# Kernel tuning notes

Hardware: AMD Instinct MI355X
Metric: run time of the kernel (lower is better)

The kernel has to match this reference:

```python
import jax, jax.numpy as jnp
import numpy as np

N, E, IN, HID, CLS = 40000, 640000, 128, 256, 40
K = 2  # SGConv k hops

def setup_inputs() -> dict:
    key = jax.random.key(0)
    ks = jax.random.split(key, 5)
    features = jax.random.normal(ks[0], (N, IN), dtype=jnp.float32)
    src = jax.random.randint(ks[1], (E,), 0, N)
    dst = jax.random.randint(ks[2], (E,), 0, N)
    # SGConv fc: in_feats -> n_hidden
    W1 = jax.random.normal(ks[3], (IN, HID), dtype=jnp.float32) / np.float32(np.sqrt(IN))
    b1 = jnp.zeros((HID,), dtype=jnp.float32)
    # model-level linear: n_hidden -> n_classes
    W2 = jax.random.normal(ks[4], (HID, CLS), dtype=jnp.float32) / np.float32(np.sqrt(HID))
    b2 = jnp.zeros((CLS,), dtype=jnp.float32)
    return {"features": features, "src": src, "dst": dst,
            "W1": W1, "b1": b1, "W2": W2, "b2": b2}

def reference(features, src, dst, W1, b1, W2, b2):
    # symmetric degree norm (DGL SGConv: in-degree, clamp min=1)
    deg = jax.ops.segment_sum(jnp.ones((E,), jnp.float32), dst, num_segments=N)
    norm = jax.lax.rsqrt(jnp.maximum(deg, 1.0))[:, None]  # [N,1]
    h = features
    for _ in range(K):
        h = h * norm
        h = jax.ops.segment_sum(h[src], dst, num_segments=N)  # A @ h via edge scatter
        h = h * norm
    h = h @ W1 + b1            # SGConv fc
    return jax.nn.relu(h) @ W2 + b2  # model relu + linear
```

## Files before the change

### kernel.cpp

```cpp
#include <hip/hip_runtime.h>

#define N_NODES 40000
#define N_EDGES 640000
#define IN_F 128
#define HID_F 256
#define CLS_F 40
#define CLS_P 48
#define MB 32
#define TS_LD 264

typedef __attribute__((ext_vector_type(8))) short bf16x8;
typedef __attribute__((ext_vector_type(4))) float f32x4;
typedef __attribute__((ext_vector_type(4))) _Float16 half4;
typedef __attribute__((ext_vector_type(8))) _Float16 half8;

#define MFMA(a, b, c) __builtin_amdgcn_mfma_f32_16x16x32_bf16(a, b, c, 0, 0, 0)

__device__ __forceinline__ unsigned short f32_to_bf16_rne(float f) {
    unsigned int u = __float_as_uint(f);
    unsigned int r = u + 0x7fffu + ((u >> 16) & 1u);
    return (unsigned short)(r >> 16);
}


__global__ void k_count(const int* __restrict__ dst, int* __restrict__ counts) {
    int e = blockIdx.x * blockDim.x + threadIdx.x;
    if (e < N_EDGES) atomicAdd(&counts[dst[e]], 1);
}

__global__ void k_scan1(const int* __restrict__ counts, int* __restrict__ bsum) {
    __shared__ int s[256];
    int i = blockIdx.x * 256 + threadIdx.x;
    s[threadIdx.x] = (i < N_NODES) ? counts[i] : 0;
    __syncthreads();
    for (int off = 128; off > 0; off >>= 1) {
        if (threadIdx.x < off) s[threadIdx.x] += s[threadIdx.x + off];
        __syncthreads();
    }
    if (threadIdx.x == 0) bsum[blockIdx.x] = s[0];
}

__global__ void k_scan2(int* __restrict__ bsum, int nb) {
    __shared__ int s[256];
    int t = threadIdx.x;
    int v = (t < nb) ? bsum[t] : 0;
    s[t] = v;
    __syncthreads();
    for (int off = 1; off < 256; off <<= 1) {
        int x = (t >= off) ? s[t - off] : 0;
        __syncthreads();
        s[t] += x;
        __syncthreads();
    }
    if (t < nb) bsum[t] = s[t] - v;
}

__global__ void k_scan3(const int* __restrict__ counts, const int* __restrict__ bsum,
                        int* __restrict__ rowptr, int* __restrict__ cursor) {
    __shared__ int s[256];
    int t = threadIdx.x;
    int i = blockIdx.x * 256 + t;
    int v = (i < N_NODES) ? counts[i] : 0;
    s[t] = v;
    __syncthreads();
    for (int off = 1; off < 256; off <<= 1) {
        int x = (t >= off) ? s[t - off] : 0;
        __syncthreads();
        s[t] += x;
        __syncthreads();
    }
    if (i < N_NODES) {
        int excl = s[t] - v + bsum[blockIdx.x];
        rowptr[i] = excl;
        cursor[i] = excl;
    }
}

__global__ void k_norm(const int* __restrict__ counts,
                       float* __restrict__ norm, float* __restrict__ norm2) {
    int i = blockIdx.x * blockDim.x + threadIdx.x;
    if (i < N_NODES) {
        float d = (float)counts[i];
        float r = rsqrtf(fmaxf(d, 1.0f));
        norm[i] = r;
        norm2[i] = r * r;
    }
}

__global__ void k_fill(const int* __restrict__ src, const int* __restrict__ dst,
                       int* __restrict__ cursor, unsigned short* __restrict__ csr_src) {
    int e = blockIdx.x * blockDim.x + threadIdx.x;
    if (e < N_EDGES) {
        int d = dst[e];
        int p = atomicAdd(&cursor[d], 1);
        csr_src[p] = (unsigned short)src[e];
    }
}


__global__ __launch_bounds__(256) void k_scale(
        const float* __restrict__ f, const float* __restrict__ norm,
        _Float16* __restrict__ xs) {
    int i = blockIdx.x * 256 + threadIdx.x;
    float s = norm[i >> 4];
    float4 a = ((const float4*)f)[i * 2];
    float4 b = ((const float4*)f)[i * 2 + 1];
    half8 h;
    h[0] = (_Float16)(a.x * s); h[1] = (_Float16)(a.y * s);
    h[2] = (_Float16)(a.z * s); h[3] = (_Float16)(a.w * s);
    h[4] = (_Float16)(b.x * s); h[5] = (_Float16)(b.y * s);
    h[6] = (_Float16)(b.z * s); h[7] = (_Float16)(b.w * s);
    ((half8*)xs)[i] = h;
}


#define HOP_GATHER16                                                          \
    int gid  = blockIdx.x * 8 + (threadIdx.x >> 5);                           \
    int lane = threadIdx.x & 31;                                              \
    if (gid >= N_NODES) return;                                               \
    int start = rowptr[gid];                                                  \
    int cnt   = counts[gid];                                                  \
    const _Float16* base = gin + lane * 4;                                    \
    float4 acc = make_float4(0.f, 0.f, 0.f, 0.f);                             \
    int i = 0;                                                                \
    for (; i + 3 < cnt; i += 4) {                                             \
        int s0 = csr_src[start + i];     int s1 = csr_src[start + i + 1];     \
        int s2 = csr_src[start + i + 2]; int s3 = csr_src[start + i + 3];     \
        half4 v0 = *(const half4*)(base + (size_t)s0 * IN_F);                 \
        half4 v1 = *(const half4*)(base + (size_t)s1 * IN_F);                 \
        half4 v2 = *(const half4*)(base + (size_t)s2 * IN_F);                 \
        half4 v3 = *(const half4*)(base + (size_t)s3 * IN_F);                 \
        acc.x += (float)v0[0] + (float)v1[0] + (float)v2[0] + (float)v3[0];   \
        acc.y += (float)v0[1] + (float)v1[1] + (float)v2[1] + (float)v3[1];   \
        acc.z += (float)v0[2] + (float)v1[2] + (float)v2[2] + (float)v3[2];   \
        acc.w += (float)v0[3] + (float)v1[3] + (float)v2[3] + (float)v3[3];   \
    }                                                                         \
    for (; i < cnt; i++) {                                                    \
        int s = csr_src[start + i];                                           \
        half4 v = *(const half4*)(base + (size_t)s * IN_F);                   \
        acc.x += (float)v[0]; acc.y += (float)v[1];                           \
        acc.z += (float)v[2]; acc.w += (float)v[3];                           \
    }

__global__ __launch_bounds__(256) void k_hop(
        const _Float16* __restrict__ gin, _Float16* __restrict__ gout,
        const unsigned short* __restrict__ csr_src, const int* __restrict__ rowptr,
        const int* __restrict__ counts, const float* __restrict__ oscale) {
    HOP_GATHER16
    float sc = oscale[gid];
    half4 o;
    o[0] = (_Float16)(acc.x * sc); o[1] = (_Float16)(acc.y * sc);
    o[2] = (_Float16)(acc.z * sc); o[3] = (_Float16)(acc.w * sc);
    *(half4*)(gout + (size_t)gid * IN_F + lane * 4) = o;
}

__global__ __launch_bounds__(256) void k_hop_split(
        const _Float16* __restrict__ gin,
        unsigned short* __restrict__ ghi, unsigned short* __restrict__ glo,
        const unsigned short* __restrict__ csr_src, const int* __restrict__ rowptr,
        const int* __restrict__ counts, const float* __restrict__ oscale) {
    HOP_GATHER16
    float sc = oscale[gid];
    float vv[4] = {acc.x * sc, acc.y * sc, acc.z * sc, acc.w * sc};
    ushort4 h, l;
    unsigned short* hp = (unsigned short*)&h;
    unsigned short* lp = (unsigned short*)&l;
    #pragma unroll
    for (int j = 0; j < 4; j++) {
        unsigned short hi = f32_to_bf16_rne(vv[j]);
        float fh = __uint_as_float((unsigned)hi << 16);
        hp[j] = hi;
        lp[j] = f32_to_bf16_rne(vv[j] - fh);
    }
    ((ushort4*)(ghi + (size_t)gid * IN_F))[lane] = h;
    ((ushort4*)(glo + (size_t)gid * IN_F))[lane] = l;
}


__global__ __launch_bounds__(256) void k_prep(
        const float* __restrict__ W1, const float* __restrict__ W2,
        unsigned short* __restrict__ w1hi, unsigned short* __restrict__ w1lo,
        unsigned short* __restrict__ w2hi, unsigned short* __restrict__ w2lo) {
    int idx = blockIdx.x * 256 + threadIdx.x;
    if (idx < IN_F * HID_F) {
        int k = idx >> 8;
        int c = idx & 255;
        float v = W1[idx];
        unsigned short hi = f32_to_bf16_rne(v);
        float fh = __uint_as_float((unsigned)hi << 16);
        unsigned short lo = f32_to_bf16_rne(v - fh);
        w1hi[c * IN_F + k] = hi;
        w1lo[c * IN_F + k] = lo;
    }
    int idx2 = idx - IN_F * HID_F;
    if (idx2 >= 0 && idx2 < CLS_P * HID_F) {
        int c = idx2 >> 8;
        int k = idx2 & 255;
        float v = (c < CLS_F) ? W2[k * CLS_F + c] : 0.f;
        unsigned short hi = f32_to_bf16_rne(v);
        float fh = __uint_as_float((unsigned)hi << 16);
        unsigned short lo = f32_to_bf16_rne(v - fh);
        w2hi[c * HID_F + k] = hi;
        w2lo[c * HID_F + k] = lo;
    }
}


#define LOAD_A(AH, AL, rt) do {                                              \
    const unsigned short* hp_ = h2hi + (size_t)(n0 + (rt) * 16 + lr) * IN_F + lg * 8; \
    const unsigned short* lp_ = h2lo + (size_t)(n0 + (rt) * 16 + lr) * IN_F + lg * 8; \
    _Pragma("unroll")                                                        \
    for (int kq = 0; kq < 4; kq++) {                                         \
        AH[kq] = *(const bf16x8*)(hp_ + kq * 32);                            \
        AL[kq] = *(const bf16x8*)(lp_ + kq * 32);                            \
    }                                                                        \
} while (0)

#define TILE(AH, AL, rt) do {                                                \
    _Pragma("unroll")                                                        \
    for (int ct = 0; ct < 4; ct++) {                                         \
        f32x4 acc = {0.f, 0.f, 0.f, 0.f};                                    \
        _Pragma("unroll")                                                    \
        for (int kq = 0; kq < 4; kq++) {                                     \
            acc = MFMA(AH[kq], b1h[ct][kq], acc);                            \
            acc = MFMA(AH[kq], b1l[ct][kq], acc);                            \
            acc = MFMA(AL[kq], b1h[ct][kq], acc);                            \
        }                                                                    \
        int col_ = w * 64 + ct * 16 + lr;                                    \
        _Pragma("unroll")                                                    \
        for (int r = 0; r < 4; r++) {                                        \
            int row_ = (rt) * 16 + lg * 4 + r;                               \
            float v_ = acc[r] + b1v[ct];                                     \
            v_ = v_ > 0.f ? v_ : 0.f;                                        \
            unsigned short hi_ = f32_to_bf16_rne(v_);                        \
            float fh_ = __uint_as_float((unsigned)hi_ << 16);                \
            tshi[row_ * TS_LD + col_] = hi_;                                 \
            tslo[row_ * TS_LD + col_] = f32_to_bf16_rne(v_ - fh_);           \
        }                                                                    \
    }                                                                        \
} while (0)

__global__ __launch_bounds__(256, 2) void k_mlp(
        const unsigned short* __restrict__ h2hi, const unsigned short* __restrict__ h2lo,
        const unsigned short* __restrict__ w1hi, const unsigned short* __restrict__ w1lo,
        const float* __restrict__ b1,
        const unsigned short* __restrict__ w2hi, const unsigned short* __restrict__ w2lo,
        const float* __restrict__ b2,
        float* __restrict__ out) {
    __shared__ __align__(16) unsigned short tshi[MB * TS_LD];
    __shared__ __align__(16) unsigned short tslo[MB * TS_LD];
    int n0 = blockIdx.x * MB;
    int t  = threadIdx.x;
    int w  = t >> 6;
    int l  = t & 63;
    int lr = l & 15;
    int lg = l >> 4;

    bf16x8 b1h[4][4], b1l[4][4];
    float  b1v[4];
    #pragma unroll
    for (int ct = 0; ct < 4; ct++) {
        int col = w * 64 + ct * 16 + lr;
        const unsigned short* bhp = w1hi + (size_t)col * IN_F + lg * 8;
        const unsigned short* blp = w1lo + (size_t)col * IN_F + lg * 8;
        #pragma unroll
        for (int kq = 0; kq < 4; kq++) {
            b1h[ct][kq] = *(const bf16x8*)(bhp + kq * 32);
            b1l[ct][kq] = *(const bf16x8*)(blp + kq * 32);
        }
        b1v[ct] = b1[col];
    }

    bf16x8 aAh[4], aAl[4], aBh[4], aBl[4];
    LOAD_A(aAh, aAl, 0);
    LOAD_A(aBh, aBl, 1);
    TILE(aAh, aAl, 0);
    TILE(aBh, aBl, 1);
    __syncthreads();

    if (w < 3) {
        int col = w * 16 + lr;
        bf16x8 b2h[8], b2l[8];
        const unsigned short* bhp = w2hi + (size_t)col * HID_F + lg * 8;
        const unsigned short* blp = w2lo + (size_t)col * HID_F + lg * 8;
        #pragma unroll
        for (int kk = 0; kk < 8; kk++) {
            b2h[kk] = *(const bf16x8*)(bhp + kk * 32);
            b2l[kk] = *(const bf16x8*)(blp + kk * 32);
        }
        float bias = (col < CLS_F) ? b2[col] : 0.f;
        #pragma unroll
        for (int rt2 = 0; rt2 < 2; rt2++) {
            const unsigned short* ahp = tshi + (rt2 * 16 + lr) * TS_LD + lg * 8;
            const unsigned short* alp = tslo + (rt2 * 16 + lr) * TS_LD + lg * 8;
            f32x4 acc0 = {0.f, 0.f, 0.f, 0.f};
            f32x4 acc1 = {0.f, 0.f, 0.f, 0.f};
            #pragma unroll
            for (int kk = 0; kk < 4; kk++) {
                bf16x8 a_h0 = *(const bf16x8*)(ahp + kk * 32);
                bf16x8 a_l0 = *(const bf16x8*)(alp + kk * 32);
                bf16x8 a_h1 = *(const bf16x8*)(ahp + (kk + 4) * 32);
                bf16x8 a_l1 = *(const bf16x8*)(alp + (kk + 4) * 32);
                acc0 = MFMA(a_h0, b2h[kk], acc0);
                acc1 = MFMA(a_h1, b2h[kk + 4], acc1);
                acc0 = MFMA(a_h0, b2l[kk], acc0);
                acc1 = MFMA(a_h1, b2l[kk + 4], acc1);
                acc0 = MFMA(a_l0, b2h[kk], acc0);
                acc1 = MFMA(a_l1, b2h[kk + 4], acc1);
            }
            if (col < CLS_F) {
                #pragma unroll
                for (int r = 0; r < 4; r++) {
                    int mrow = n0 + rt2 * 16 + lg * 4 + r;
                    out[(size_t)mrow * CLS_F + col] = acc0[r] + acc1[r] + bias;
                }
            }
        }
    }
}


extern "C" void kernel_launch(void* const* d_in, const int* in_sizes, int n_in,
                              void* d_out, int out_size, void* d_ws, size_t ws_size,
                              hipStream_t stream) {
    const float* features = (const float*)d_in[0];
    const int*   src      = (const int*)d_in[1];
    const int*   dst      = (const int*)d_in[2];
    const float* W1       = (const float*)d_in[3];
    const float* b1       = (const float*)d_in[4];
    const float* W2       = (const float*)d_in[5];
    const float* b2       = (const float*)d_in[6];
    float*       out      = (float*)d_out;

    char* ws = (char*)d_ws;
    size_t off = 0;
    auto alloc = [&](size_t bytes) -> void* {
        void* p = ws + off;
        off += (bytes + 255) & ~(size_t)255;
        return p;
    };
    int*   counts = (int*)alloc((size_t)N_NODES * 4);
    int*   rowptr = (int*)alloc((size_t)N_NODES * 4);
    int*   cursor = (int*)alloc((size_t)N_NODES * 4);
    int*   bsum   = (int*)alloc(256 * 4);
    float* norm   = (float*)alloc((size_t)N_NODES * 4);
    float* norm2  = (float*)alloc((size_t)N_NODES * 4);
    unsigned short* csr = (unsigned short*)alloc((size_t)N_EDGES * 2);
    _Float16* xs  = (_Float16*)alloc((size_t)N_NODES * IN_F * 2);
    _Float16* h1  = (_Float16*)alloc((size_t)N_NODES * IN_F * 2);
    unsigned short* h2hi = (unsigned short*)alloc((size_t)N_NODES * IN_F * 2);
    unsigned short* h2lo = (unsigned short*)alloc((size_t)N_NODES * IN_F * 2);
    unsigned short* w1hi = (unsigned short*)alloc((size_t)HID_F * IN_F * 2);
    unsigned short* w1lo = (unsigned short*)alloc((size_t)HID_F * IN_F * 2);
    unsigned short* w2hi = (unsigned short*)alloc((size_t)CLS_P * HID_F * 2);
    unsigned short* w2lo = (unsigned short*)alloc((size_t)CLS_P * HID_F * 2);

    hipMemsetAsync(counts, 0, (size_t)N_NODES * 4, stream);

    int nb = (N_NODES + 255) / 256;
    k_count<<<(N_EDGES + 255) / 256, 256, 0, stream>>>(dst, counts);
    k_prep<<<(IN_F * HID_F + CLS_P * HID_F + 255) / 256, 256, 0, stream>>>(
        W1, W2, w1hi, w1lo, w2hi, w2lo);
    k_scan1<<<nb, 256, 0, stream>>>(counts, bsum);
    k_scan2<<<1, 256, 0, stream>>>(bsum, nb);
    k_scan3<<<nb, 256, 0, stream>>>(counts, bsum, rowptr, cursor);
    k_norm<<<nb, 256, 0, stream>>>(counts, norm, norm2);
    k_fill<<<(N_EDGES + 255) / 256, 256, 0, stream>>>(src, dst, cursor, csr);

    k_scale<<<N_NODES * IN_F / 8 / 256, 256, 0, stream>>>(features, norm, xs);
    k_hop<<<(N_NODES + 7) / 8, 256, 0, stream>>>(xs, h1, csr, rowptr, counts, norm2);
    k_hop_split<<<(N_NODES + 7) / 8, 256, 0, stream>>>(h1, h2hi, h2lo, csr, rowptr,
                                                       counts, norm);

    k_mlp<<<N_NODES / MB, 256, 0, stream>>>(h2hi, h2lo, w1hi, w1lo, b1, w2hi, w2lo, b2, out);
}
```

Before: 237.6 us.

## Fuse second hop gather into MLP kernel and merge setup kernels

The second hop's gather and hi/lo bf16 split now run inside the MLP kernel. Results go to a swizzled LDS tile instead of round-tripping h2hi/h2lo through global memory. The norm computation is folded into the scan kernel, and edge fill, feature scaling and weight prep are merged into one multi-role launch. This removes several launches and about 20 MB of intermediate traffic. The risk is that the latency-bound gather now runs inside the MFMA kernel, which has higher register and LDS pressure and lower occupancy.

After: 262.5 us. 10.5% more time.

```diff
diff --git a/kernel.cpp b/kernel.cpp
--- a/kernel.cpp
+++ b/kernel.cpp
@@ -8,6 +8,7 @@
 #define CLS_P 48
 #define MB 32
 #define TS_LD 264
+#define A_LD 136
 
 typedef __attribute__((ext_vector_type(8))) short bf16x8;
 typedef __attribute__((ext_vector_type(4))) float f32x4;
@@ -20,6 +21,10 @@
     unsigned int u = __float_as_uint(f);
     unsigned int r = u + 0x7fffu + ((u >> 16) & 1u);
     return (unsigned short)(r >> 16);
+}
+
+__device__ __forceinline__ int aswz(int row, int col_us) {
+    return row * A_LD + (col_us ^ ((row & 7) << 3));
 }
 
 
@@ -55,8 +60,9 @@
     if (t < nb) bsum[t] = s[t] - v;
 }
 
-__global__ void k_scan3(const int* __restrict__ counts, const int* __restrict__ bsum,
-                        int* __restrict__ rowptr, int* __restrict__ cursor) {
+__global__ void k_scan3n(const int* __restrict__ counts, const int* __restrict__ bsum,
+                         int* __restrict__ rowptr, int* __restrict__ cursor,
+                         float* __restrict__ norm, float* __restrict__ norm2) {
     __shared__ int s[256];
     int t = threadIdx.x;
     int i = blockIdx.x * 256 + t;
@@ -73,80 +79,94 @@
         int excl = s[t] - v + bsum[blockIdx.x];
         rowptr[i] = excl;
         cursor[i] = excl;
-    }
-}
-
-__global__ void k_norm(const int* __restrict__ counts,
-                       float* __restrict__ norm, float* __restrict__ norm2) {
-    int i = blockIdx.x * blockDim.x + threadIdx.x;
-    if (i < N_NODES) {
-        float d = (float)counts[i];
+        float d = (float)v;
         float r = rsqrtf(fmaxf(d, 1.0f));
         norm[i] = r;
         norm2[i] = r * r;
     }
 }
 
-__global__ void k_fill(const int* __restrict__ src, const int* __restrict__ dst,
-                       int* __restrict__ cursor, unsigned short* __restrict__ csr_src) {
-    int e = blockIdx.x * blockDim.x + threadIdx.x;
-    if (e < N_EDGES) {
+
+__global__ __launch_bounds__(256) void k_fsp(
+        const int* __restrict__ src, const int* __restrict__ dst,
+        int* __restrict__ cursor, unsigned short* __restrict__ csr_src,
+        const float* __restrict__ features, const float* __restrict__ norm,
+        _Float16* __restrict__ xs,
+        const float* __restrict__ W1, const float* __restrict__ W2,
+        unsigned short* __restrict__ w1hi, unsigned short* __restrict__ w1lo,
+        unsigned short* __restrict__ w2hi, unsigned short* __restrict__ w2lo) {
+    int b = blockIdx.x;
+    if (b < 2500) {
+        int e = b * 256 + threadIdx.x;
         int d = dst[e];
         int p = atomicAdd(&cursor[d], 1);
         csr_src[p] = (unsigned short)src[e];
-    }
-}
-
-
-__global__ __launch_bounds__(256) void k_scale(
-        const float* __restrict__ f, const float* __restrict__ norm,
-        _Float16* __restrict__ xs) {
-    int i = blockIdx.x * 256 + threadIdx.x;
-    float s = norm[i >> 4];
-    float4 a = ((const float4*)f)[i * 2];
-    float4 b = ((const float4*)f)[i * 2 + 1];
-    half8 h;
-    h[0] = (_Float16)(a.x * s); h[1] = (_Float16)(a.y * s);
-    h[2] = (_Float16)(a.z * s); h[3] = (_Float16)(a.w * s);
-    h[4] = (_Float16)(b.x * s); h[5] = (_Float16)(b.y * s);
-    h[6] = (_Float16)(b.z * s); h[7] = (_Float16)(b.w * s);
-    ((half8*)xs)[i] = h;
-}
-
-
-#define HOP_GATHER16                                                          \
-    int gid  = blockIdx.x * 8 + (threadIdx.x >> 5);                           \
-    int lane = threadIdx.x & 31;                                              \
-    if (gid >= N_NODES) return;                                               \
-    int start = rowptr[gid];                                                  \
-    int cnt   = counts[gid];                                                  \
-    const _Float16* base = gin + lane * 4;                                    \
-    float4 acc = make_float4(0.f, 0.f, 0.f, 0.f);                             \
-    int i = 0;                                                                \
-    for (; i + 3 < cnt; i += 4) {                                             \
-        int s0 = csr_src[start + i];     int s1 = csr_src[start + i + 1];     \
-        int s2 = csr_src[start + i + 2]; int s3 = csr_src[start + i + 3];     \
-        half4 v0 = *(const half4*)(base + (size_t)s0 * IN_F);                 \
-        half4 v1 = *(const half4*)(base + (size_t)s1 * IN_F);                 \
-        half4 v2 = *(const half4*)(base + (size_t)s2 * IN_F);                 \
-        half4 v3 = *(const half4*)(base + (size_t)s3 * IN_F);                 \
-        acc.x += (float)v0[0] + (float)v1[0] + (float)v2[0] + (float)v3[0];   \
-        acc.y += (float)v0[1] + (float)v1[1] + (float)v2[1] + (float)v3[1];   \
-        acc.z += (float)v0[2] + (float)v1[2] + (float)v2[2] + (float)v3[2];   \
-        acc.w += (float)v0[3] + (float)v1[3] + (float)v2[3] + (float)v3[3];   \
-    }                                                                         \
-    for (; i < cnt; i++) {                                                    \
-        int s = csr_src[start + i];                                           \
-        half4 v = *(const half4*)(base + (size_t)s * IN_F);                   \
-        acc.x += (float)v[0]; acc.y += (float)v[1];                           \
-        acc.z += (float)v[2]; acc.w += (float)v[3];                           \
-    }
+    } else if (b < 5000) {
+        int i = (b - 2500) * 256 + threadIdx.x;
+        float s = norm[i >> 4];
+        float4 a = ((const float4*)features)[i * 2];
+        float4 c = ((const float4*)features)[i * 2 + 1];
+        half8 h;
+        h[0] = (_Float16)(a.x * s); h[1] = (_Float16)(a.y * s);
+        h[2] = (_Float16)(a.z * s); h[3] = (_Float16)(a.w * s);
+        h[4] = (_Float16)(c.x * s); h[5] = (_Float16)(c.y * s);
+        h[6] = (_Float16)(c.z * s); h[7] = (_Float16)(c.w * s);
+        ((half8*)xs)[i] = h;
+    } else {
+        int idx = (b - 5000) * 256 + threadIdx.x;
+        if (idx < IN_F * HID_F) {
+            int k = idx >> 8;
+            int c = idx & 255;
+            float v = W1[idx];
+            unsigned short hi = f32_to_bf16_rne(v);
+            float fh = __uint_as_float((unsigned)hi << 16);
+            w1hi[c * IN_F + k] = hi;
+            w1lo[c * IN_F + k] = f32_to_bf16_rne(v - fh);
+        }
+        int idx2 = idx - IN_F * HID_F;
+        if (idx2 >= 0 && idx2 < CLS_P * HID_F) {
+            int c = idx2 >> 8;
+            int k = idx2 & 255;
+            float v = (c < CLS_F) ? W2[k * CLS_F + c] : 0.f;
+            unsigned short hi = f32_to_bf16_rne(v);
+            float fh = __uint_as_float((unsigned)hi << 16);
+            w2hi[c * HID_F + k] = hi;
+            w2lo[c * HID_F + k] = f32_to_bf16_rne(v - fh);
+        }
+    }
+}
+
 
 __global__ __launch_bounds__(256) void k_hop(
         const _Float16* __restrict__ gin, _Float16* __restrict__ gout,
         const unsigned short* __restrict__ csr_src, const int* __restrict__ rowptr,
         const int* __restrict__ counts, const float* __restrict__ oscale) {
-    HOP_GATHER16
+    int gid  = blockIdx.x * 8 + (threadIdx.x >> 5);
+    int lane = threadIdx.x & 31;
+    if (gid >= N_NODES) return;
+    int start = rowptr[gid];
+    int cnt   = counts[gid];
+    const _Float16* base = gin + lane * 4;
+    float4 acc = make_float4(0.f, 0.f, 0.f, 0.f);
+    int i = 0;
+    for (; i + 3 < cnt; i += 4) {
+        int s0 = csr_src[start + i];     int s1 = csr_src[start + i + 1];
+        int s2 = csr_src[start + i + 2]; int s3 = csr_src[start + i + 3];
+        half4 v0 = *(const half4*)(base + (size_t)s0 * IN_F);
+        half4 v1 = *(const half4*)(base + (size_t)s1 * IN_F);
+        half4 v2 = *(const half4*)(base + (size_t)s2 * IN_F);
+        half4 v3 = *(const half4*)(base + (size_t)s3 * IN_F);
+        acc.x += (float)v0[0] + (float)v1[0] + (float)v2[0] + (float)v3[0];
+        acc.y += (float)v0[1] + (float)v1[1] + (float)v2[1] + (float)v3[1];
+        acc.z += (float)v0[2] + (float)v1[2] + (float)v2[2] + (float)v3[2];
+        acc.w += (float)v0[3] + (float)v1[3] + (float)v2[3] + (float)v3[3];
+    }
+    for (; i < cnt; i++) {
+        int s = csr_src[start + i];
+        half4 v = *(const half4*)(base + (size_t)s * IN_F);
+        acc.x += (float)v[0]; acc.y += (float)v[1];
+        acc.z += (float)v[2]; acc.w += (float)v[3];
+    }
     float sc = oscale[gid];
     half4 o;
     o[0] = (_Float16)(acc.x * sc); o[1] = (_Float16)(acc.y * sc);
@@ -154,99 +174,18 @@
     *(half4*)(gout + (size_t)gid * IN_F + lane * 4) = o;
 }
 
-__global__ __launch_bounds__(256) void k_hop_split(
-        const _Float16* __restrict__ gin,
-        unsigned short* __restrict__ ghi, unsigned short* __restrict__ glo,
+
+__global__ __launch_bounds__(256, 2) void k_mlp(
+        const _Float16* __restrict__ h1,
         const unsigned short* __restrict__ csr_src, const int* __restrict__ rowptr,
-        const int* __restrict__ counts, const float* __restrict__ oscale) {
-    HOP_GATHER16
-    float sc = oscale[gid];
-    float vv[4] = {acc.x * sc, acc.y * sc, acc.z * sc, acc.w * sc};
-    ushort4 h, l;
-    unsigned short* hp = (unsigned short*)&h;
-    unsigned short* lp = (unsigned short*)&l;
-    #pragma unroll
-    for (int j = 0; j < 4; j++) {
-        unsigned short hi = f32_to_bf16_rne(vv[j]);
-        float fh = __uint_as_float((unsigned)hi << 16);
-        hp[j] = hi;
-        lp[j] = f32_to_bf16_rne(vv[j] - fh);
-    }
-    ((ushort4*)(ghi + (size_t)gid * IN_F))[lane] = h;
-    ((ushort4*)(glo + (size_t)gid * IN_F))[lane] = l;
-}
-
-
-__global__ __launch_bounds__(256) void k_prep(
-        const float* __restrict__ W1, const float* __restrict__ W2,
-        unsigned short* __restrict__ w1hi, unsigned short* __restrict__ w1lo,
-        unsigned short* __restrict__ w2hi, unsigned short* __restrict__ w2lo) {
-    int idx = blockIdx.x * 256 + threadIdx.x;
-    if (idx < IN_F * HID_F) {
-        int k = idx >> 8;
-        int c = idx & 255;
-        float v = W1[idx];
-        unsigned short hi = f32_to_bf16_rne(v);
-        float fh = __uint_as_float((unsigned)hi << 16);
-        unsigned short lo = f32_to_bf16_rne(v - fh);
-        w1hi[c * IN_F + k] = hi;
-        w1lo[c * IN_F + k] = lo;
-    }
-    int idx2 = idx - IN_F * HID_F;
-    if (idx2 >= 0 && idx2 < CLS_P * HID_F) {
-        int c = idx2 >> 8;
-        int k = idx2 & 255;
-        float v = (c < CLS_F) ? W2[k * CLS_F + c] : 0.f;
-        unsigned short hi = f32_to_bf16_rne(v);
-        float fh = __uint_as_float((unsigned)hi << 16);
-        unsigned short lo = f32_to_bf16_rne(v - fh);
-        w2hi[c * HID_F + k] = hi;
-        w2lo[c * HID_F + k] = lo;
-    }
-}
-
-
-#define LOAD_A(AH, AL, rt) do {                                              \
-    const unsigned short* hp_ = h2hi + (size_t)(n0 + (rt) * 16 + lr) * IN_F + lg * 8; \
-    const unsigned short* lp_ = h2lo + (size_t)(n0 + (rt) * 16 + lr) * IN_F + lg * 8; \
-    _Pragma("unroll")                                                        \
-    for (int kq = 0; kq < 4; kq++) {                                         \
-        AH[kq] = *(const bf16x8*)(hp_ + kq * 32);                            \
-        AL[kq] = *(const bf16x8*)(lp_ + kq * 32);                            \
-    }                                                                        \
-} while (0)
-
-#define TILE(AH, AL, rt) do {                                                \
-    _Pragma("unroll")                                                        \
-    for (int ct = 0; ct < 4; ct++) {                                         \
-        f32x4 acc = {0.f, 0.f, 0.f, 0.f};                                    \
-        _Pragma("unroll")                                                    \
-        for (int kq = 0; kq < 4; kq++) {                                     \
-            acc = MFMA(AH[kq], b1h[ct][kq], acc);                            \
-            acc = MFMA(AH[kq], b1l[ct][kq], acc);                            \
-            acc = MFMA(AL[kq], b1h[ct][kq], acc);                            \
-        }                                                                    \
-        int col_ = w * 64 + ct * 16 + lr;                                    \
-        _Pragma("unroll")                                                    \
-        for (int r = 0; r < 4; r++) {                                        \
-            int row_ = (rt) * 16 + lg * 4 + r;                               \
-            float v_ = acc[r] + b1v[ct];                                     \
-            v_ = v_ > 0.f ? v_ : 0.f;                                        \
-            unsigned short hi_ = f32_to_bf16_rne(v_);                        \
-            float fh_ = __uint_as_float((unsigned)hi_ << 16);                \
-            tshi[row_ * TS_LD + col_] = hi_;                                 \
-            tslo[row_ * TS_LD + col_] = f32_to_bf16_rne(v_ - fh_);           \
-        }                                                                    \
-    }                                                                        \
-} while (0)
-
-__global__ __launch_bounds__(256, 2) void k_mlp(
-        const unsigned short* __restrict__ h2hi, const unsigned short* __restrict__ h2lo,
+        const int* __restrict__ counts, const float* __restrict__ norm,
         const unsigned short* __restrict__ w1hi, const unsigned short* __restrict__ w1lo,
         const float* __restrict__ b1,
         const unsigned short* __restrict__ w2hi, const unsigned short* __restrict__ w2lo,
         const float* __restrict__ b2,
         float* __restrict__ out) {
+    __shared__ __align__(16) unsigned short ahi[MB * A_LD];
+    __shared__ __align__(16) unsigned short alo[MB * A_LD];
     __shared__ __align__(16) unsigned short tshi[MB * TS_LD];
     __shared__ __align__(16) unsigned short tslo[MB * TS_LD];
     int n0 = blockIdx.x * MB;
@@ -271,11 +210,84 @@
         b1v[ct] = b1[col];
     }
 
-    bf16x8 aAh[4], aAl[4], aBh[4], aBl[4];
-    LOAD_A(aAh, aAl, 0);
-    LOAD_A(aBh, aBl, 1);
-    TILE(aAh, aAl, 0);
-    TILE(aBh, aBl, 1);
+    {
+        int grp  = t >> 5;
+        int lane = t & 31;
+        for (int nn = grp; nn < MB; nn += 8) {
+            int gid = n0 + nn;
+            int start = rowptr[gid];
+            int cnt   = counts[gid];
+            const _Float16* base = h1 + lane * 4;
+            float4 acc = make_float4(0.f, 0.f, 0.f, 0.f);
+            int i = 0;
+            for (; i + 3 < cnt; i += 4) {
+                int s0 = csr_src[start + i];     int s1 = csr_src[start + i + 1];
+                int s2 = csr_src[start + i + 2]; int s3 = csr_src[start + i + 3];
+                half4 v0 = *(const half4*)(base + (size_t)s0 * IN_F);
+                half4 v1 = *(const half4*)(base + (size_t)s1 * IN_F);
+                half4 v2 = *(const half4*)(base + (size_t)s2 * IN_F);
+                half4 v3 = *(const half4*)(base + (size_t)s3 * IN_F);
+                acc.x += (float)v0[0] + (float)v1[0] + (float)v2[0] + (float)v3[0];
+                acc.y += (float)v0[1] + (float)v1[1] + (float)v2[1] + (float)v3[1];
+                acc.z += (float)v0[2] + (float)v1[2] + (float)v2[2] + (float)v3[2];
+                acc.w += (float)v0[3] + (float)v1[3] + (float)v2[3] + (float)v3[3];
+            }
+            for (; i < cnt; i++) {
+                int s = csr_src[start + i];
+                half4 v = *(const half4*)(base + (size_t)s * IN_F);
+                acc.x += (float)v[0]; acc.y += (float)v[1];
+                acc.z += (float)v[2]; acc.w += (float)v[3];
+            }
+            float sc = norm[gid];
+            float vv[4] = {acc.x * sc, acc.y * sc, acc.z * sc, acc.w * sc};
+            ushort4 h, lo4;
+            unsigned short* hp = (unsigned short*)&h;
+            unsigned short* lp = (unsigned short*)&lo4;
+            #pragma unroll
+            for (int j = 0; j < 4; j++) {
+                unsigned short hi = f32_to_bf16_rne(vv[j]);
+                float fh = __uint_as_float((unsigned)hi << 16);
+                hp[j] = hi;
+                lp[j] = f32_to_bf16_rne(vv[j] - fh);
+            }
+            int o = aswz(nn, lane * 4);
+            *(ushort4*)&ahi[o] = h;
+            *(ushort4*)&alo[o] = lo4;
+        }
+    }
+    __syncthreads();
+
+    #pragma unroll
+    for (int rt = 0; rt < 2; rt++) {
+        bf16x8 aH[4], aL[4];
+        #pragma unroll
+        for (int kq = 0; kq < 4; kq++) {
+            int o = aswz(rt * 16 + lr, (kq * 4 + lg) * 8);
+            aH[kq] = *(const bf16x8*)&ahi[o];
+            aL[kq] = *(const bf16x8*)&alo[o];
+        }
+        #pragma unroll
+        for (int ct = 0; ct < 4; ct++) {
+            f32x4 acc = {0.f, 0.f, 0.f, 0.f};
+            #pragma unroll
+            for (int kq = 0; kq < 4; kq++) {
+                acc = MFMA(aH[kq], b1h[ct][kq], acc);
+                acc = MFMA(aH[kq], b1l[ct][kq], acc);
+                acc = MFMA(aL[kq], b1h[ct][kq], acc);
+            }
+            int col = w * 64 + ct * 16 + lr;
+            #pragma unroll
+            for (int r = 0; r < 4; r++) {
+                int row = rt * 16 + lg * 4 + r;
+                float v = acc[r] + b1v[ct];
+                v = v > 0.f ? v : 0.f;
+                unsigned short hi = f32_to_bf16_rne(v);
+                float fh = __uint_as_float((unsigned)hi << 16);
+                tshi[row * TS_LD + col] = hi;
+                tslo[row * TS_LD + col] = f32_to_bf16_rne(v - fh);
+            }
+        }
+    }
     __syncthreads();
 
     if (w < 3) {
@@ -348,8 +360,6 @@
     unsigned short* csr = (unsigned short*)alloc((size_t)N_EDGES * 2);
     _Float16* xs  = (_Float16*)alloc((size_t)N_NODES * IN_F * 2);
     _Float16* h1  = (_Float16*)alloc((size_t)N_NODES * IN_F * 2);
-    unsigned short* h2hi = (unsigned short*)alloc((size_t)N_NODES * IN_F * 2);
-    unsigned short* h2lo = (unsigned short*)alloc((size_t)N_NODES * IN_F * 2);
     unsigned short* w1hi = (unsigned short*)alloc((size_t)HID_F * IN_F * 2);
     unsigned short* w1lo = (unsigned short*)alloc((size_t)HID_F * IN_F * 2);
     unsigned short* w2hi = (unsigned short*)alloc((size_t)CLS_P * HID_F * 2);
@@ -359,18 +369,15 @@
 
     int nb = (N_NODES + 255) / 256;
     k_count<<<(N_EDGES + 255) / 256, 256, 0, stream>>>(dst, counts);
-    k_prep<<<(IN_F * HID_F + CLS_P * HID_F + 255) / 256, 256, 0, stream>>>(
-        W1, W2, w1hi, w1lo, w2hi, w2lo);
     k_scan1<<<nb, 256, 0, stream>>>(counts, bsum);
     k_scan2<<<1, 256, 0, stream>>>(bsum, nb);
-    k_scan3<<<nb, 256, 0, stream>>>(counts, bsum, rowptr, cursor);
-    k_norm<<<nb, 256, 0, stream>>>(counts, norm, norm2);
-    k_fill<<<(N_EDGES + 255) / 256, 256, 0, stream>>>(src, dst, cursor, csr);
-
-    k_scale<<<N_NODES * IN_F / 8 / 256, 256, 0, stream>>>(features, norm, xs);
+    k_scan3n<<<nb, 256, 0, stream>>>(counts, bsum, rowptr, cursor, norm, norm2);
+
+    int prep_blocks = (IN_F * HID_F + CLS_P * HID_F + 255) / 256;
+    k_fsp<<<5000 + prep_blocks, 256, 0, stream>>>(
+        src, dst, cursor, csr, features, norm, xs, W1, W2, w1hi, w1lo, w2hi, w2lo);
+
     k_hop<<<(N_NODES + 7) / 8, 256, 0, stream>>>(xs, h1, csr, rowptr, counts, norm2);
-    k_hop_split<<<(N_NODES + 7) / 8, 256, 0, stream>>>(h1, h2hi, h2lo, csr, rowptr,
-                                                       counts, norm);
-
-    k_mlp<<<N_NODES / MB, 256, 0, stream>>>(h2hi, h2lo, w1hi, w1lo, b1, w2hi, w2lo, b2, out);
-}
+    k_mlp<<<N_NODES / MB, 256, 0, stream>>>(h1, csr, rowptr, counts, norm,
+                                            w1hi, w1lo, b1, w2hi, w2lo, b2, out);
+}
```

## Fuse CSR scan, norm, fill, scale and weight prep into fewer kernels

Applied to the files above, without the earlier changes.

Replaces the three-kernel prefix scan with a single scan that grabs each block's base offset through a global atomic counter, and computes the degree norms in the same kernel. CSR fill, feature scaling and weight bf16 splitting are merged into one block-partitioned kernel. The goal is to cut kernel launch count and the serial gaps between small preprocessing kernels. Row offsets now follow atomic arrival order instead of node order; this stays correct because each row's range is still contiguous.

After: 227.8 us. 1.04x faster.

```diff
diff --git a/kernel.cpp b/kernel.cpp
--- a/kernel.cpp
+++ b/kernel.cpp
@@ -23,41 +23,18 @@
 }
 
 
-__global__ void k_count(const int* __restrict__ dst, int* __restrict__ counts) {
+__global__ void k_count(const int* __restrict__ dst, int* __restrict__ counts,
+                        int* __restrict__ gcur) {
     int e = blockIdx.x * blockDim.x + threadIdx.x;
+    if (e == 0) *gcur = 0;
     if (e < N_EDGES) atomicAdd(&counts[dst[e]], 1);
 }
 
-__global__ void k_scan1(const int* __restrict__ counts, int* __restrict__ bsum) {
+__global__ void k_scanA(const int* __restrict__ counts, int* __restrict__ gcur,
+                        int* __restrict__ rowptr, int* __restrict__ cursor,
+                        float* __restrict__ norm, float* __restrict__ norm2) {
     __shared__ int s[256];
-    int i = blockIdx.x * 256 + threadIdx.x;
-    s[threadIdx.x] = (i < N_NODES) ? counts[i] : 0;
-    __syncthreads();
-    for (int off = 128; off > 0; off >>= 1) {
-        if (threadIdx.x < off) s[threadIdx.x] += s[threadIdx.x + off];
-        __syncthreads();
-    }
-    if (threadIdx.x == 0) bsum[blockIdx.x] = s[0];
-}
-
-__global__ void k_scan2(int* __restrict__ bsum, int nb) {
-    __shared__ int s[256];
-    int t = threadIdx.x;
-    int v = (t < nb) ? bsum[t] : 0;
-    s[t] = v;
-    __syncthreads();
-    for (int off = 1; off < 256; off <<= 1) {
-        int x = (t >= off) ? s[t - off] : 0;
-        __syncthreads();
-        s[t] += x;
-        __syncthreads();
-    }
-    if (t < nb) bsum[t] = s[t] - v;
-}
-
-__global__ void k_scan3(const int* __restrict__ counts, const int* __restrict__ bsum,
-                        int* __restrict__ rowptr, int* __restrict__ cursor) {
-    __shared__ int s[256];
+    __shared__ int base;
     int t = threadIdx.x;
     int i = blockIdx.x * 256 + t;
     int v = (i < N_NODES) ? counts[i] : 0;
@@ -69,48 +46,66 @@
         s[t] += x;
         __syncthreads();
     }
+    if (t == 255) base = atomicAdd(gcur, s[255]);
+    __syncthreads();
     if (i < N_NODES) {
-        int excl = s[t] - v + bsum[blockIdx.x];
+        int excl = base + s[t] - v;
         rowptr[i] = excl;
         cursor[i] = excl;
-    }
-}
-
-__global__ void k_norm(const int* __restrict__ counts,
-                       float* __restrict__ norm, float* __restrict__ norm2) {
-    int i = blockIdx.x * blockDim.x + threadIdx.x;
-    if (i < N_NODES) {
-        float d = (float)counts[i];
-        float r = rsqrtf(fmaxf(d, 1.0f));
+        float r = rsqrtf(fmaxf((float)v, 1.0f));
         norm[i] = r;
         norm2[i] = r * r;
     }
 }
 
-__global__ void k_fill(const int* __restrict__ src, const int* __restrict__ dst,
-                       int* __restrict__ cursor, unsigned short* __restrict__ csr_src) {
-    int e = blockIdx.x * blockDim.x + threadIdx.x;
-    if (e < N_EDGES) {
+
+__global__ __launch_bounds__(256) void k_fsp(
+        const int* __restrict__ src, const int* __restrict__ dst,
+        int* __restrict__ cursor, unsigned short* __restrict__ csr_src,
+        const float* __restrict__ features, const float* __restrict__ norm,
+        _Float16* __restrict__ xs,
+        const float* __restrict__ W1, const float* __restrict__ W2,
+        unsigned short* __restrict__ w1hi, unsigned short* __restrict__ w1lo,
+        unsigned short* __restrict__ w2hi, unsigned short* __restrict__ w2lo) {
+    int b = blockIdx.x;
+    if (b < 2500) {
+        int e = b * 256 + threadIdx.x;
         int d = dst[e];
         int p = atomicAdd(&cursor[d], 1);
         csr_src[p] = (unsigned short)src[e];
-    }
-}
-
-
-__global__ __launch_bounds__(256) void k_scale(
-        const float* __restrict__ f, const float* __restrict__ norm,
-        _Float16* __restrict__ xs) {
-    int i = blockIdx.x * 256 + threadIdx.x;
-    float s = norm[i >> 4];
-    float4 a = ((const float4*)f)[i * 2];
-    float4 b = ((const float4*)f)[i * 2 + 1];
-    half8 h;
-    h[0] = (_Float16)(a.x * s); h[1] = (_Float16)(a.y * s);
-    h[2] = (_Float16)(a.z * s); h[3] = (_Float16)(a.w * s);
-    h[4] = (_Float16)(b.x * s); h[5] = (_Float16)(b.y * s);
-    h[6] = (_Float16)(b.z * s); h[7] = (_Float16)(b.w * s);
-    ((half8*)xs)[i] = h;
+    } else if (b < 5000) {
+        int i = (b - 2500) * 256 + threadIdx.x;
+        float s = norm[i >> 4];
+        float4 a = ((const float4*)features)[i * 2];
+        float4 c = ((const float4*)features)[i * 2 + 1];
+        half8 h;
+        h[0] = (_Float16)(a.x * s); h[1] = (_Float16)(a.y * s);
+        h[2] = (_Float16)(a.z * s); h[3] = (_Float16)(a.w * s);
+        h[4] = (_Float16)(c.x * s); h[5] = (_Float16)(c.y * s);
+        h[6] = (_Float16)(c.z * s); h[7] = (_Float16)(c.w * s);
+        ((half8*)xs)[i] = h;
+    } else {
+        int idx = (b - 5000) * 256 + threadIdx.x;
+        if (idx < IN_F * HID_F) {
+            int k = idx >> 8;
+            int c = idx & 255;
+            float v = W1[idx];
+            unsigned short hi = f32_to_bf16_rne(v);
+            float fh = __uint_as_float((unsigned)hi << 16);
+            w1hi[c * IN_F + k] = hi;
+            w1lo[c * IN_F + k] = f32_to_bf16_rne(v - fh);
+        }
+        int idx2 = idx - IN_F * HID_F;
+        if (idx2 >= 0 && idx2 < CLS_P * HID_F) {
+            int c = idx2 >> 8;
+            int k = idx2 & 255;
+            float v = (c < CLS_F) ? W2[k * CLS_F + c] : 0.f;
+            unsigned short hi = f32_to_bf16_rne(v);
+            float fh = __uint_as_float((unsigned)hi << 16);
+            w2hi[c * HID_F + k] = hi;
+            w2lo[c * HID_F + k] = f32_to_bf16_rne(v - fh);
+        }
+    }
 }
 
 
@@ -174,35 +169,6 @@
     }
     ((ushort4*)(ghi + (size_t)gid * IN_F))[lane] = h;
     ((ushort4*)(glo + (size_t)gid * IN_F))[lane] = l;
-}
-
-
-__global__ __launch_bounds__(256) void k_prep(
-        const float* __restrict__ W1, const float* __restrict__ W2,
-        unsigned short* __restrict__ w1hi, unsigned short* __restrict__ w1lo,
-        unsigned short* __restrict__ w2hi, unsigned short* __restrict__ w2lo) {
-    int idx = blockIdx.x * 256 + threadIdx.x;
-    if (idx < IN_F * HID_F) {
-        int k = idx >> 8;
-        int c = idx & 255;
-        float v = W1[idx];
-        unsigned short hi = f32_to_bf16_rne(v);
-        float fh = __uint_as_float((unsigned)hi << 16);
-        unsigned short lo = f32_to_bf16_rne(v - fh);
-        w1hi[c * IN_F + k] = hi;
-        w1lo[c * IN_F + k] = lo;
-    }
-    int idx2 = idx - IN_F * HID_F;
-    if (idx2 >= 0 && idx2 < CLS_P * HID_F) {
-        int c = idx2 >> 8;
-        int k = idx2 & 255;
-        float v = (c < CLS_F) ? W2[k * CLS_F + c] : 0.f;
-        unsigned short hi = f32_to_bf16_rne(v);
-        float fh = __uint_as_float((unsigned)hi << 16);
-        unsigned short lo = f32_to_bf16_rne(v - fh);
-        w2hi[c * HID_F + k] = hi;
-        w2lo[c * HID_F + k] = lo;
-    }
 }
 
 
@@ -340,9 +306,9 @@
         return p;
     };
     int*   counts = (int*)alloc((size_t)N_NODES * 4);
+    int*   gcur   = (int*)alloc(256);
     int*   rowptr = (int*)alloc((size_t)N_NODES * 4);
     int*   cursor = (int*)alloc((size_t)N_NODES * 4);
-    int*   bsum   = (int*)alloc(256 * 4);
     float* norm   = (float*)alloc((size_t)N_NODES * 4);
     float* norm2  = (float*)alloc((size_t)N_NODES * 4);
     unsigned short* csr = (unsigned short*)alloc((size_t)N_EDGES * 2);
@@ -358,16 +324,13 @@
     hipMemsetAsync(counts, 0, (size_t)N_NODES * 4, stream);
 
     int nb = (N_NODES + 255) / 256;
-    k_count<<<(N_EDGES + 255) / 256, 256, 0, stream>>>(dst, counts);
-    k_prep<<<(IN_F * HID_F + CLS_P * HID_F + 255) / 256, 256, 0, stream>>>(
-        W1, W2, w1hi, w1lo, w2hi, w2lo);
-    k_scan1<<<nb, 256, 0, stream>>>(counts, bsum);
-    k_scan2<<<1, 256, 0, stream>>>(bsum, nb);
-    k_scan3<<<nb, 256, 0, stream>>>(counts, bsum, rowptr, cursor);
-    k_norm<<<nb, 256, 0, stream>>>(counts, norm, norm2);
-    k_fill<<<(N_EDGES + 255) / 256, 256, 0, stream>>>(src, dst, cursor, csr);
-
-    k_scale<<<N_NODES * IN_F / 8 / 256, 256, 0, stream>>>(features, norm, xs);
+    k_count<<<(N_EDGES + 255) / 256, 256, 0, stream>>>(dst, counts, gcur);
+    k_scanA<<<nb, 256, 0, stream>>>(counts, gcur, rowptr, cursor, norm, norm2);
+
+    int prep_blocks = (IN_F * HID_F + CLS_P * HID_F + 255) / 256;
+    k_fsp<<<5000 + prep_blocks, 256, 0, stream>>>(
+        src, dst, cursor, csr, features, norm, xs, W1, W2, w1hi, w1lo, w2hi, w2lo);
+
     k_hop<<<(N_NODES + 7) / 8, 256, 0, stream>>>(xs, h1, csr, rowptr, counts, norm2);
     k_hop_split<<<(N_NODES + 7) / 8, 256, 0, stream>>>(h1, h2hi, h2lo, csr, rowptr,
                                                        counts, norm);
```
